# Optimization experiments

Hardware: AMD Instinct MI355X
Metric: run time of the kernel (lower is better)

Reference implementation:

```python
import jax, jax.numpy as jnp
import numpy as np

EPS = 1e-8


def eq_linear(z, weight, bias):
    # EqualisedLinear: runtime weight scale c = 1/sqrt(in_features)
    c = 1.0 / np.sqrt(weight.shape[1]).astype(np.float32)
    return z @ (weight * c).T + bias


def mod_conv(x, w_raw, s, demodulate):
    # w_raw: [out, in, k, k], s: [b, in]
    out_c, in_c, k, _ = w_raw.shape
    c = 1.0 / np.sqrt(in_c * k * k).astype(np.float32)
    wt = w_raw * c
    # per-sample modulated weights: [b, out, in, k, k]
    ws = wt[None] * s[:, None, :, None, None]
    if demodulate:
        sigma_inv = jax.lax.rsqrt(jnp.sum(ws * ws, axis=(2, 3, 4), keepdims=True) + EPS)
        ws = ws * sigma_inv
    def conv1(xi, wi):
        return jax.lax.conv_general_dilated(
            xi[None], wi, window_strides=(1, 1), padding='SAME',
            dimension_numbers=('NCHW', 'OIHW', 'NCHW'))[0]
    return jax.vmap(conv1)(x, ws)


def lrelu(v):
    return jax.nn.leaky_relu(v, 0.2)


def style_block(x, w, noise, style_w, style_b, conv_w, noise_scale, bias):
    s = eq_linear(w, style_w, style_b)
    x = mod_conv(x, conv_w, s, demodulate=True)
    x = x + noise_scale[None, :, None, None] * noise
    return lrelu(x + bias[None, :, None, None])


def to_rgb(x, w, style_w, style_b, conv_w, bias):
    s = eq_linear(w, style_w, style_b)
    x = mod_conv(x, conv_w, s, demodulate=False)
    return lrelu(x + bias[None, :, None, None])


def setup_inputs() -> dict:
    key = jax.random.key(0)
    ks = jax.random.split(key, 16)
    B, C, H, W = 16, 512, 64, 64
    D = 512
    OUT = 3
    return {
        'x': jax.random.normal(ks[0], (B, C, H, W), jnp.float32),
        'w': jax.random.normal(ks[1], (B, D), jnp.float32),
        'noise1': jax.random.normal(ks[2], (B, 1, H, W), jnp.float32),
        'noise2': jax.random.normal(ks[3], (B, 1, H, W), jnp.float32),
        'sb1_style_w': jax.random.normal(ks[4], (C, D), jnp.float32),
        'sb1_style_b': jnp.ones((C,), jnp.float32),
        'sb1_conv_w': jax.random.normal(ks[5], (C, C, 3, 3), jnp.float32),
        'sb1_noise_scale': 0.1 * jax.random.normal(ks[6], (1,), jnp.float32),
        'sb1_bias': 0.1 * jax.random.normal(ks[7], (C,), jnp.float32),
        'sb2_style_w': jax.random.normal(ks[8], (C, D), jnp.float32),
        'sb2_style_b': jnp.ones((C,), jnp.float32),
        'sb2_conv_w': jax.random.normal(ks[9], (C, C, 3, 3), jnp.float32),
        'sb2_noise_scale': 0.1 * jax.random.normal(ks[10], (1,), jnp.float32),
        'sb2_bias': 0.1 * jax.random.normal(ks[11], (C,), jnp.float32),
        'rgb_style_w': jax.random.normal(ks[12], (C, D), jnp.float32),
        'rgb_style_b': jnp.ones((C,), jnp.float32),
        'rgb_conv_w': jax.random.normal(ks[13], (OUT, C, 1, 1), jnp.float32),
        'rgb_bias': 0.1 * jax.random.normal(ks[14], (OUT,), jnp.float32),
    }


def reference(x, w, noise1, noise2,
              sb1_style_w, sb1_style_b, sb1_conv_w, sb1_noise_scale, sb1_bias,
              sb2_style_w, sb2_style_b, sb2_conv_w, sb2_noise_scale, sb2_bias,
              rgb_style_w, rgb_style_b, rgb_conv_w, rgb_bias):
    x = style_block(x, w, noise1, sb1_style_w, sb1_style_b, sb1_conv_w, sb1_noise_scale, sb1_bias)
    x = style_block(x, w, noise2, sb2_style_w, sb2_style_b, sb2_conv_w, sb2_noise_scale, sb2_bias)
    rgb = to_rgb(x, w, rgb_style_w, rgb_style_b, rgb_conv_w, rgb_bias)
    return (x, rgb)
```

## Files before the change

### kernel.cpp

```cpp
#include <hip/hip_runtime.h>
#include <hip/hip_bf16.h>

typedef float f32x4 __attribute__((ext_vector_type(4)));
typedef short short8 __attribute__((ext_vector_type(8)));

#define CC    512
#define PIX   4096
#define ROWB  4224
#define TILE6 25344
#define TILE4 16896

__device__ __forceinline__ unsigned short f2bf(float f){
    __hip_bfloat16 h = __float2bfloat16(f);
    return __builtin_bit_cast(unsigned short, h);
}
__device__ __forceinline__ unsigned pk2(float a, float b){
    return (unsigned)f2bf(a) | ((unsigned)f2bf(b) << 16);
}
__device__ __forceinline__ void mfma_bf16(f32x4& c, short8 a, short8 b){
    asm("v_mfma_f32_16x16x32_bf16 %0, %1, %2, %0" : "+v"(c) : "v"(a), "v"(b));
}
__device__ __forceinline__ void gl_lds16(const void* g, void* l){
    __builtin_amdgcn_global_load_lds(
        (const __attribute__((address_space(1))) unsigned int*)g,
        (__attribute__((address_space(3))) unsigned int*)l, 16, 0, 0);
}

__global__ void k_style3(const float* __restrict__ w,
                         const float* __restrict__ sw0, const float* __restrict__ sb0, float* __restrict__ o0,
                         const float* __restrict__ sw1, const float* __restrict__ sb1, float* __restrict__ o1,
                         const float* __restrict__ sw2, const float* __restrict__ sb2, float* __restrict__ o2){
    __shared__ float wl[512];
    const int b = blockIdx.x, l = blockIdx.y, tid = threadIdx.x;
    const float* sw = (l==0) ? sw0 : (l==1 ? sw1 : sw2);
    const float* sb = (l==0) ? sb0 : (l==1 ? sb1 : sb2);
    float* so       = (l==0) ? o0  : (l==1 ? o1  : o2);
    wl[tid]       = w[b*512 + tid];
    wl[tid + 256] = w[b*512 + 256 + tid];
    __syncthreads();
    const float c = 0.044194173824159216f;
    for (int cc = tid; cc < 512; cc += 256){
        const float4* row = (const float4*)(sw + cc*512);
        float acc = 0.f;
        #pragma unroll 4
        for (int dd = 0; dd < 128; ++dd){
            float4 v = row[dd];
            float4 wv = ((const float4*)wl)[dd];
            acc += v.x*wv.x + v.y*wv.y + v.z*wv.z + v.w*wv.w;
        }
        so[b*512 + cc] = acc * c + sb[cc];
    }
}

__global__ void k_w2(const float* __restrict__ cw1, const float* __restrict__ cw2,
                     float* __restrict__ w2_1, float* __restrict__ w2_2){
    int gid = blockIdx.x*256 + threadIdx.x;
    int layer = gid >> 18; int r = gid & 262143;
    const float* cw = layer ? cw2 : cw1;
    float* w2 = layer ? w2_2 : w2_1;
    const float c2 = 1.0f/4608.0f;
    const float* p = cw + r*9;
    float sum = 0.f;
    #pragma unroll
    for (int t=0;t<9;++t){ float v = p[t]; sum += v*v; }
    w2[r] = sum * c2;
}

__global__ void k_demod2(const float* __restrict__ w21, const float* __restrict__ w22,
                         const float* __restrict__ s1,  const float* __restrict__ s2,
                         float* __restrict__ d1, float* __restrict__ d2){
    __shared__ float s2l[512];
    const int b = blockIdx.x, l = blockIdx.y, o = threadIdx.x;
    const float* w2 = l ? w22 : w21;
    const float* s  = l ? s2  : s1;
    float* d        = l ? d2  : d1;
    float sv = s[b*512 + o]; s2l[o] = sv*sv;
    __syncthreads();
    const float4* row = (const float4*)(w2 + o*512);
    const float4* sq  = (const float4*)s2l;
    float acc = 0.f;
    #pragma unroll 4
    for (int i=0;i<128;++i){
        float4 a = row[i], bq = sq[i];
        acc += a.x*bq.x + a.y*bq.y + a.z*bq.z + a.w*bq.w;
    }
    d[b*512 + o] = rsqrtf(acc + 1e-8f);
}

__global__ void k_pack(const float* __restrict__ cw1, const float* __restrict__ cw2,
                       uint4* __restrict__ wpk1, uint4* __restrict__ wpk2){
    int gid = blockIdx.x*256 + threadIdx.x;
    int layer = (gid >= 294912);
    int r = layer ? gid - 294912 : gid;
    const float* cw = layer ? cw2 : cw1;
    uint4* dst = layer ? wpk2 : wpk1;
    int lane = r & 63;
    int ofr  = (r>>6) & 31;
    int cb   = (r>>11) & 15;
    int t    = r>>15;
    int o  = ofr*16 + (lane&15);
    int i0 = cb*32 + (lane>>4)*8;
    const float c = 0.014731391274719738f;
    const float* src = cw + (o*512 + i0)*9 + t;
    float f[8];
    #pragma unroll
    for (int j=0;j<8;++j) f[j] = src[j*9]*c;
    uint4 wv;
    wv.x = pk2(f[0],f[1]); wv.y = pk2(f[2],f[3]);
    wv.z = pk2(f[4],f[5]); wv.w = pk2(f[6],f[7]);
    dst[r] = wv;
}

__global__ void k_stage_g(const float* __restrict__ x, const float* __restrict__ s,
                          char* __restrict__ xpg){
    const int tid = threadIdx.x;
    const int cb = blockIdx.x, rb = blockIdx.y, b = blockIdx.z;
    const int r0 = rb*4;
    const int scol   = tid & 63;
    const int schunk = (tid>>6) & 3;
    unsigned wcol = (unsigned)((scol+1)*64 + schunk*16);
    wcol ^= (unsigned)((((scol+1)>>1)&3)<<4);
    float sv[8];
    const float* sp8 = s + b*512 + cb*32 + schunk*8;
    #pragma unroll
    for (int j=0;j<8;++j) sv[j] = sp8[j];
    char* dst = xpg + ((size_t)((b*16 + rb)*16 + cb))*TILE6;
    const float* srcbase = x + (size_t)b*(512*PIX) + (size_t)(cb*32 + schunk*8)*PIX + scol;
    #pragma unroll
    for (int row=0; row<6; ++row){
        int gr = r0 - 1 + row;
        uint4 wq = make_uint4(0u,0u,0u,0u);
        if (0 <= gr && gr < 64){
            const float* sp = srcbase + gr*64;
            float f0 = sp[0*PIX]*sv[0], f1 = sp[1*PIX]*sv[1];
            float f2 = sp[2*PIX]*sv[2], f3 = sp[3*PIX]*sv[3];
            float f4 = sp[4*PIX]*sv[4], f5 = sp[5*PIX]*sv[5];
            float f6 = sp[6*PIX]*sv[6], f7 = sp[7*PIX]*sv[7];
            wq.x = pk2(f0,f1); wq.y = pk2(f2,f3);
            wq.z = pk2(f4,f5); wq.w = pk2(f6,f7);
        }
        *(uint4*)(dst + row*ROWB + wcol) = wq;
    }
    if (tid < 48){
        int row = tid>>3; int hc = (tid&4) ? 65 : 0; int ck = tid&3;
        unsigned a = (unsigned)((row*66 + hc)*64 + ck*16);
        a ^= (unsigned)(((hc>>1)&3)<<4);
        *(uint4*)(dst + a) = make_uint4(0u,0u,0u,0u);
    }
}

__global__ __launch_bounds__(256, 2)
void k_conv(const char* __restrict__ xpg, float* __restrict__ y,
            const unsigned short* __restrict__ wpk,
            const float* __restrict__ dmod, const float* __restrict__ noise,
            const float* __restrict__ nsp, const float* __restrict__ bias){
    __shared__ __align__(16) char smem[2*TILE4];
    char* xh0 = smem;
    char* xh1 = smem + TILE4;

    const int tid  = threadIdx.x;
    const int obp  = blockIdx.x;
    const int rb   = blockIdx.y;
    const int b    = blockIdx.z;
    const int r0   = rb*2;
    const int lane = tid & 63;
    const int wv   = tid >> 6;
    const int ln15 = lane & 15;
    const int hi   = lane >> 4;

    f32x4 acc[4][8];
    #pragma unroll
    for (int mi=0;mi<4;++mi)
        #pragma unroll
        for (int ni=0;ni<8;++ni) acc[mi][ni] = (f32x4)(0.f);

    unsigned bcol[3][4];
    #pragma unroll
    for (int dxi=0; dxi<3; ++dxi)
        #pragma unroll
        for (int ni=0; ni<4; ++ni){
            int xcol = ni*16 + ln15 + dxi;
            unsigned a = (unsigned)(xcol*64 + hi*16);
            a ^= (unsigned)(((xcol>>1)&3)<<4);
            bcol[dxi][ni] = a;
        }

    const char* tbase = xpg + ((size_t)((b*16 + (rb>>1))*16))*TILE6
                            + (size_t)(rb&1)*2*ROWB;
    auto stage = [&](int cb2, char* dstb){
        const char* src = tbase + (size_t)cb2*TILE6;
        #pragma unroll
        for (int k=0;k<4;++k)
            gl_lds16(src + (size_t)(tid + k*256)*16, dstb + (tid + k*256)*16);
        if (tid < 32)
            gl_lds16(src + (size_t)(1024 + tid)*16, dstb + (1024 + tid)*16);
    };

    stage(0, xh0);

    const short8* wpf = (const short8*)wpk + (size_t)(obp*16 + wv*4)*64 + lane;

    #pragma unroll 2
    for (int cb=0; cb<16; ++cb){
        __syncthreads();
        const short8* wp = wpf + (size_t)cb*(32*64);
        short8 Af[4];
        #pragma unroll
        for (int mi=0;mi<4;++mi) Af[mi] = wp[mi*64];
        if (cb+1 < 16) stage(cb+1, (cb&1) ? xh0 : xh1);
        const char* cur = (cb&1) ? xh1 : xh0;
        #pragma unroll
        for (int t=0; t<9; ++t){
            const int dxi = t%3;
            if (t > 0){
                #pragma unroll
                for (int mi=0;mi<4;++mi) Af[mi] = wp[(size_t)t*(16*32*64) + mi*64];
            }
            const char* rbase0 = cur + (t/3)*ROWB;
            const char* rbase1 = rbase0 + ROWB;
            short8 Bf[8];
            #pragma unroll
            for (int ni=0;ni<4;++ni) Bf[ni]   = *(const short8*)(rbase0 + bcol[dxi][ni]);
            #pragma unroll
            for (int ni=0;ni<4;++ni) Bf[4+ni] = *(const short8*)(rbase1 + bcol[dxi][ni]);
            #pragma unroll
            for (int ni=0;ni<8;++ni)
                #pragma unroll
                for (int mi=0;mi<4;++mi)
                    mfma_bf16(acc[mi][ni], Af[mi], Bf[ni]);
        }
    }

    const int obase = obp*256 + wv*64;
    const float nsv = nsp[0];
    const float* dgl = dmod + b*512 + obase;
    const float* bgl = bias + obase;
    float nz[8];
    #pragma unroll
    for (int ni=0;ni<8;++ni){
        int row = r0 + (ni>>2);
        nz[ni] = nsv * noise[b*PIX + row*64 + (ni&3)*16 + ln15];
    }
    float* yb = y + ((size_t)(b*512 + obase))*PIX;
    #pragma unroll
    for (int mi=0;mi<4;++mi){
        float dv[4], bv[4];
        #pragma unroll
        for (int r=0;r<4;++r){
            int ol = mi*16 + hi*4 + r;
            dv[r] = dgl[ol]; bv[r] = bgl[ol];
        }
        #pragma unroll
        for (int ni=0;ni<8;++ni){
            int row = r0 + (ni>>2);
            int col = (ni&3)*16 + ln15;
            #pragma unroll
            for (int r=0;r<4;++r){
                float v = acc[mi][ni][r]*dv[r] + nz[ni] + bv[r];
                v = fmaxf(v, 0.2f*v);
                yb[(size_t)(mi*16 + hi*4 + r)*PIX + row*64 + col] = v;
            }
        }
    }
}

__global__ void k_rgb(const float* __restrict__ x2, const float* __restrict__ srgb,
                      const float* __restrict__ cw, const float* __restrict__ bias,
                      float* __restrict__ out){
    __shared__ float4 wr[512];
    const int b = blockIdx.x, tid = threadIdx.x;
    const float c = 0.044194173824159216f;
    for (int cc = tid; cc < 512; cc += 256){
        float sc = srgb[b*512 + cc]*c;
        wr[cc] = make_float4(cw[cc]*sc, cw[512+cc]*sc, cw[1024+cc]*sc, 0.f);
    }
    __syncthreads();
    int px = blockIdx.y*256 + tid;
    const float* xp = x2 + (size_t)b*(512*PIX) + px;
    float a0=0.f, a1=0.f, a2=0.f;
    #pragma unroll 4
    for (int i=0;i<512;++i){
        float xv = xp[(size_t)i*PIX];
        float4 wv = wr[i];
        a0 += wv.x*xv; a1 += wv.y*xv; a2 += wv.z*xv;
    }
    a0 += bias[0]; a1 += bias[1]; a2 += bias[2];
    out[(size_t)(b*3+0)*PIX + px] = fmaxf(a0, 0.2f*a0);
    out[(size_t)(b*3+1)*PIX + px] = fmaxf(a1, 0.2f*a1);
    out[(size_t)(b*3+2)*PIX + px] = fmaxf(a2, 0.2f*a2);
}

extern "C" void kernel_launch(void* const* d_in, const int* in_sizes, int n_in,
                              void* d_out, int out_size, void* d_ws, size_t ws_size,
                              hipStream_t stream) {
    const float* x    = (const float*)d_in[0];
    const float* w    = (const float*)d_in[1];
    const float* n1   = (const float*)d_in[2];
    const float* n2   = (const float*)d_in[3];
    const float* s1w  = (const float*)d_in[4];
    const float* s1b  = (const float*)d_in[5];
    const float* c1w  = (const float*)d_in[6];
    const float* ns1  = (const float*)d_in[7];
    const float* b1   = (const float*)d_in[8];
    const float* s2w  = (const float*)d_in[9];
    const float* s2b  = (const float*)d_in[10];
    const float* c2w  = (const float*)d_in[11];
    const float* ns2  = (const float*)d_in[12];
    const float* b2   = (const float*)d_in[13];
    const float* rw   = (const float*)d_in[14];
    const float* rbv  = (const float*)d_in[15];
    const float* rcw  = (const float*)d_in[16];
    const float* rbias= (const float*)d_in[17];

    float* out_x   = (float*)d_out;
    float* out_rgb = out_x + (size_t)16*512*PIX;

    char* ws = (char*)d_ws;
    float* s1   = (float*)(ws + 0);
    float* s2   = (float*)(ws + 32768);
    float* srgb = (float*)(ws + 65536);
    float* d1   = (float*)(ws + 98304);
    float* d2   = (float*)(ws + 131072);
    float* w21  = (float*)(ws + 163840);
    float* w22  = (float*)(ws + 163840 + 1048576);
    unsigned short* wp1 = (unsigned short*)(ws + 2260992);
    unsigned short* wp2 = wp1 + 2359296;
    char* xpg   = ws + 11698176;
    float* x1   = out_x;

    k_style3<<<dim3(16,3), 256, 0, stream>>>(w, s1w, s1b, s1, s2w, s2b, s2, rw, rbv, srgb);
    k_w2<<<2048, 256, 0, stream>>>(c1w, c2w, w21, w22);
    k_pack<<<2304, 256, 0, stream>>>(c1w, c2w, (uint4*)wp1, (uint4*)wp2);
    k_demod2<<<dim3(16,2), 512, 0, stream>>>(w21, w22, s1, s2, d1, d2);

    dim3 cg(2, 32, 16);
    k_stage_g<<<dim3(16,16,16), 256, 0, stream>>>(x, s1, xpg);
    k_conv<<<cg, 256, 0, stream>>>(xpg, x1, wp1, d1, n1, ns1, b1);
    k_stage_g<<<dim3(16,16,16), 256, 0, stream>>>(x1, s2, xpg);
    k_conv<<<cg, 256, 0, stream>>>(xpg, out_x, wp2, d2, n2, ns2, b2);
    k_rgb<<<dim3(16,16), 256, 0, stream>>>(out_x, srgb, rcw, rbias, out_rgb);
}
```

Measured before the change: 765.8 us.

## Fuse second-stage input staging into first conv epilogue via packed bf16 output

The first conv's epilogue now multiplies by the next block's style, converts to bf16, and writes directly into the padded, swizzled tile layout (including halo row duplicates) that the second conv reads. This removes the fp32 intermediate write and the separate staging kernel pass. A small kernel zeroes the halo columns and the boundary rows. The path needs a larger workspace, guarded by a size check, and otherwise falls back to the old sequence. The scattered 8-byte stores with duplicated halo rows may be less coalesced than the original stores.

Result: slower. 808.4 us (+5.6%).

```diff
diff --git a/kernel.cpp b/kernel.cpp
--- a/kernel.cpp
+++ b/kernel.cpp
@@ -149,11 +149,33 @@
     }
 }
 
+__global__ void k_zero(char* __restrict__ xpg){
+    const int tile = blockIdx.x;
+    const int RB = (tile>>4) & 15;
+    char* base = xpg + (size_t)tile*TILE6;
+    const int tid = threadIdx.x;
+    if (tid < 48){
+        int row = tid>>3; int hc = (tid&4) ? 65 : 0; int ck = tid&3;
+        bool skip = (RB==0 && row==0) || (RB==15 && row==5);
+        if (!skip){
+            unsigned a = (unsigned)((row*66 + hc)*64 + ck*16);
+            a ^= (unsigned)(((hc>>1)&3)<<4);
+            *(uint4*)(base + a) = make_uint4(0u,0u,0u,0u);
+        }
+    }
+    if (RB == 0)
+        for (int i=tid; i<264; i+=256) *(uint4*)(base + i*16) = make_uint4(0u,0u,0u,0u);
+    if (RB == 15)
+        for (int i=tid; i<264; i+=256) *(uint4*)(base + 5*ROWB + i*16) = make_uint4(0u,0u,0u,0u);
+}
+
+template<bool PACKOUT>
 __global__ __launch_bounds__(256, 2)
 void k_conv(const char* __restrict__ xpg, float* __restrict__ y,
             const unsigned short* __restrict__ wpk,
             const float* __restrict__ dmod, const float* __restrict__ noise,
-            const float* __restrict__ nsp, const float* __restrict__ bias){
+            const float* __restrict__ nsp, const float* __restrict__ bias,
+            const float* __restrict__ snext, char* __restrict__ ypk){
     __shared__ __align__(16) char smem[2*TILE4];
     char* xh0 = smem;
     char* xh1 = smem + TILE4;
@@ -241,24 +263,65 @@
         int row = r0 + (ni>>2);
         nz[ni] = nsv * noise[b*PIX + row*64 + (ni&3)*16 + ln15];
     }
-    float* yb = y + ((size_t)(b*512 + obase))*PIX;
-    #pragma unroll
-    for (int mi=0;mi<4;++mi){
-        float dv[4], bv[4];
-        #pragma unroll
-        for (int r=0;r<4;++r){
-            int ol = mi*16 + hi*4 + r;
-            dv[r] = dgl[ol]; bv[r] = bgl[ol];
-        }
-        #pragma unroll
-        for (int ni=0;ni<8;++ni){
-            int row = r0 + (ni>>2);
-            int col = (ni&3)*16 + ln15;
+    if (PACKOUT){
+        #pragma unroll
+        for (int mi=0;mi<4;++mi){
+            float dv[4], bv[4], sv2[4];
             #pragma unroll
             for (int r=0;r<4;++r){
-                float v = acc[mi][ni][r]*dv[r] + nz[ni] + bv[r];
-                v = fmaxf(v, 0.2f*v);
-                yb[(size_t)(mi*16 + hi*4 + r)*PIX + row*64 + col] = v;
+                int ol = mi*16 + hi*4 + r;
+                dv[r] = dgl[ol]; bv[r] = bgl[ol];
+                sv2[r] = snext[b*512 + obase + ol];
+            }
+            const int cbt = (obase + mi*16) >> 5;
+            const unsigned coff = (unsigned)(((mi&1)*2 + (hi>>1))*16);
+            const unsigned hoff = (unsigned)((hi&1)*8);
+            #pragma unroll
+            for (int ni=0;ni<8;++ni){
+                int row = r0 + (ni>>2);
+                int col = (ni&3)*16 + ln15;
+                float p[4];
+                #pragma unroll
+                for (int r=0;r<4;++r){
+                    float v = acc[mi][ni][r]*dv[r] + nz[ni] + bv[r];
+                    v = fmaxf(v, 0.2f*v);
+                    p[r] = v * sv2[r];
+                }
+                uint2 wq; wq.x = pk2(p[0],p[1]); wq.y = pk2(p[2],p[3]);
+                unsigned wordoff = ((unsigned)((col+1)*64) + coff)
+                                 ^ ((((unsigned)(col+1)>>1)&3)<<4);
+                unsigned inoff = wordoff + hoff;
+                int RBa = (row+1)>>2, tra = (row+1)&3;
+                if (RBa <= 15){
+                    size_t tb = ((size_t)((b*16+RBa)*16 + cbt))*TILE6 + (size_t)tra*ROWB;
+                    *(uint2*)(ypk + tb + inoff) = wq;
+                }
+                if (tra <= 1 && RBa >= 1){
+                    size_t tb = ((size_t)((b*16+RBa-1)*16 + cbt))*TILE6 + (size_t)(tra+4)*ROWB;
+                    *(uint2*)(ypk + tb + inoff) = wq;
+                }
+            }
+        }
+    } else {
+        float* yb = y + ((size_t)(b*512 + obase))*PIX;
+        #pragma unroll
+        for (int mi=0;mi<4;++mi){
+            float dv[4], bv[4];
+            #pragma unroll
+            for (int r=0;r<4;++r){
+                int ol = mi*16 + hi*4 + r;
+                dv[r] = dgl[ol]; bv[r] = bgl[ol];
+            }
+            #pragma unroll
+            for (int ni=0;ni<8;++ni){
+                int row = r0 + (ni>>2);
+                int col = (ni&3)*16 + ln15;
+                #pragma unroll
+                for (int r=0;r<4;++r){
+                    float v = acc[mi][ni][r]*dv[r] + nz[ni] + bv[r];
+                    v = fmaxf(v, 0.2f*v);
+                    yb[(size_t)(mi*16 + hi*4 + r)*PIX + row*64 + col] = v;
+                }
             }
         }
     }
@@ -325,8 +388,9 @@
     float* w22  = (float*)(ws + 163840 + 1048576);
     unsigned short* wp1 = (unsigned short*)(ws + 2260992);
     unsigned short* wp2 = wp1 + 2359296;
-    char* xpg   = ws + 11698176;
-    float* x1   = out_x;
+    char* xpg1  = ws + 11698176;
+    char* xpg2  = xpg1 + 103809024;
+    const bool fused = (ws_size >= (size_t)219316224);
 
     k_style3<<<dim3(16,3), 256, 0, stream>>>(w, s1w, s1b, s1, s2w, s2b, s2, rw, rbv, srgb);
     k_w2<<<2048, 256, 0, stream>>>(c1w, c2w, w21, w22);
@@ -334,9 +398,16 @@
     k_demod2<<<dim3(16,2), 512, 0, stream>>>(w21, w22, s1, s2, d1, d2);
 
     dim3 cg(2, 32, 16);
-    k_stage_g<<<dim3(16,16,16), 256, 0, stream>>>(x, s1, xpg);
-    k_conv<<<cg, 256, 0, stream>>>(xpg, x1, wp1, d1, n1, ns1, b1);
-    k_stage_g<<<dim3(16,16,16), 256, 0, stream>>>(x1, s2, xpg);
-    k_conv<<<cg, 256, 0, stream>>>(xpg, out_x, wp2, d2, n2, ns2, b2);
+    k_stage_g<<<dim3(16,16,16), 256, 0, stream>>>(x, s1, xpg1);
+    if (fused){
+        k_zero<<<4096, 256, 0, stream>>>(xpg2);
+        k_conv<true ><<<cg, 256, 0, stream>>>(xpg1, nullptr, wp1, d1, n1, ns1, b1, s2, xpg2);
+        k_conv<false><<<cg, 256, 0, stream>>>(xpg2, out_x, wp2, d2, n2, ns2, b2, nullptr, nullptr);
+    } else {
+        float* x1 = out_x;
+        k_conv<false><<<cg, 256, 0, stream>>>(xpg1, x1, wp1, d1, n1, ns1, b1, nullptr, nullptr);
+        k_stage_g<<<dim3(16,16,16), 256, 0, stream>>>(x1, s2, xpg1);
+        k_conv<false><<<cg, 256, 0, stream>>>(xpg1, out_x, wp2, d2, n2, ns2, b2, nullptr, nullptr);
+    }
     k_rgb<<<dim3(16,16), 256, 0, stream>>>(out_x, srgb, rcw, rbias, out_rgb);
 }
```
